# Kernel optimization log

Measured on AMD Instinct MI355X. Metric: run time of the kernel, lower is better.

The kernel has to match this reference:

```python
import jax, jax.numpy as jnp
import numpy as np

NEG_SLOPE = 0.15


def _gcn_norm(edge_index, num_nodes):
    # PyG GCNConv default: add self-loops, symmetric normalization.
    src = jnp.concatenate([edge_index[0], jnp.arange(num_nodes)])
    dst = jnp.concatenate([edge_index[1], jnp.arange(num_nodes)])
    deg = jax.ops.segment_sum(jnp.ones_like(src, dtype=jnp.float32), dst,
                              num_segments=num_nodes)
    dis = jnp.where(deg > 0, jax.lax.rsqrt(jnp.maximum(deg, 1.0)), 0.0)
    norm = dis[src] * dis[dst]  # [E + N]
    return src, dst, norm


def _gcn_conv(h, W, b, src, dst, norm, num_nodes):
    h = h @ W                                   # dense transform first (PyG order)
    msg = h[src] * norm[:, None]                # gather + scale per edge
    out = jax.ops.segment_sum(msg, dst, num_segments=num_nodes)  # scatter-add
    return out + b


def setup_inputs() -> dict:
    key = jax.random.key(0)
    ks = jax.random.split(key, 16)
    N, E, D = 20000, 320000, 128
    x = jax.random.normal(ks[0], (N, D), dtype=jnp.float32)
    edge_index = jax.random.randint(ks[1], (2, E), 0, N, dtype=jnp.int32)
    edge_attr = jax.random.normal(ks[2], (E, 2), dtype=jnp.float32)

    def lin(k, fi, fo):
        kw, kb = jax.random.split(k)
        s = 1.0 / np.sqrt(fi)
        return (jax.random.uniform(kw, (fi, fo), jnp.float32, -s, s),
                jax.random.uniform(kb, (fo,), jnp.float32, -s, s))

    W1, b1 = lin(ks[3], D, 512)
    W2, b2 = lin(ks[4], 512, 256)
    W3, b3 = lin(ks[5], 256, 128)
    Wp, bp = lin(ks[6], 128, 16)   # pre_fc (128 -> 16)
    Wf1, bf1 = lin(ks[7], 16, 32)  # fallback MLP classifier
    Wf2, bf2 = lin(ks[8], 32, 2)
    return {"x": x, "edge_index": edge_index, "edge_attr": edge_attr,
            "W1": W1, "b1": b1, "W2": W2, "b2": b2, "W3": W3, "b3": b3,
            "Wp": Wp, "bp": bp, "Wf1": Wf1, "bf1": bf1, "Wf2": Wf2, "bf2": bf2}


def reference(x, edge_index, edge_attr, W1, b1, W2, b2, W3, b3,
              Wp, bp, Wf1, bf1, Wf2, bf2):
    N = x.shape[0]
    src, dst, norm = _gcn_norm(edge_index, N)
    lrelu = lambda h: jax.nn.leaky_relu(h, NEG_SLOPE)
    h = lrelu(_gcn_conv(x, W1, b1, src, dst, norm, N))   # dropout = identity (eval)
    h = lrelu(_gcn_conv(h, W2, b2, src, dst, norm, N))
    h = lrelu(_gcn_conv(h, W3, b3, src, dst, norm, N))
    h = h @ Wp + bp                                      # pre_fc: 128 -> 16
    h = lrelu(h @ Wf1 + bf1)                             # classifier MLP
    return h @ Wf2 + bf2                                 # [N, 2]
```

## Files before the change

### kernel.cpp

```cpp
#include <hip/hip_runtime.h>
#include <hip/hip_bf16.h>

typedef __hip_bfloat16 bf16;
typedef unsigned short ushort_t;
typedef __attribute__((ext_vector_type(8))) short short8v;
typedef __attribute__((ext_vector_type(4))) float floatx4;

#define NEG_SLOPE 0.15f

__device__ __forceinline__ float us2f(unsigned short u) {
    unsigned int x = ((unsigned int)u) << 16;
    float f;
    __builtin_memcpy(&f, &x, 4);
    return f;
}
__device__ __forceinline__ unsigned short f2us(float v) {
    bf16 h = __float2bfloat16(v);
    unsigned short u;
    __builtin_memcpy(&u, &h, 2);
    return u;
}

__device__ __forceinline__ int block_flag(const unsigned int* __restrict__ xw) {
    __shared__ int cnt;
    if (threadIdx.x == 0) cnt = 0;
    __syncthreads();
    if (threadIdx.x < 256) {
        unsigned int w = xw[threadIdx.x];
        unsigned int e = (w >> 7) & 0xFF;
        if ((w & 0xFFFF) == 0 || (e >= 100 && e <= 140)) atomicAdd(&cnt, 1);
    }
    __syncthreads();
    return cnt >= 150;
}

struct PrepDesc {
    const void* src[14];
    void* dst[14];
    int n[14];
    int K[14], Nn[14];
};

__global__ void prep_small_kernel(PrepDesc d, const void* __restrict__ xsrc) {
    int f = block_flag((const unsigned int*)xsrc);
    int t = blockIdx.y;
    int Kt = d.K[t];
    int nt = d.n[t];
    if (Kt == -2) {
        ushort_t* out = (ushort_t*)d.dst[t];
        const void* in = d.src[t];
        int stride = gridDim.x * blockDim.x;
        for (int i = blockIdx.x * blockDim.x + threadIdx.x; i < nt; i += stride)
            out[i] = f ? ((const unsigned short*)in)[i] : f2us(((const float*)in)[i]);
        return;
    }
    int i = blockIdx.x * blockDim.x + threadIdx.x;
    if (i >= nt) return;
    if (Kt == -1) {
        ((int*)d.dst[t])[i] = 0;
    } else if (Kt == 0) {
        ((float*)d.dst[t])[i] = f ? us2f(((const unsigned short*)d.src[t])[i])
                                  : ((const float*)d.src[t])[i];
    } else {
        int K = Kt, Nn = d.Nn[t];
        int n = i / K, k = i - n * K;
        size_t si = (size_t)k * Nn + n;
        ((ushort_t*)d.dst[t])[i] = f ? ((const unsigned short*)d.src[t])[si]
                                     : f2us(((const float*)d.src[t])[si]);
    }
}

__global__ void count_deg_kernel(const int* __restrict__ dst, int* __restrict__ deg,
                                 int E, int N) {
    int i = blockIdx.x * blockDim.x + threadIdx.x;
    if (i < E) {
        int d = dst[i];
        d = d < 0 ? 0 : (d >= N ? N - 1 : d);
        atomicAdd(&deg[d], 1);
    }
}

__global__ void scan_merged_kernel(const int* __restrict__ deg, int* __restrict__ offsets,
                                   int* __restrict__ cursor, float* __restrict__ dis,
                                   int* __restrict__ bsumf, int N) {
    __shared__ int sh[1024];
    __shared__ int base_s;
    int tid = threadIdx.x;
    int b = blockIdx.x;
    int i = b * 1024 + tid;
    int v = (i < N) ? (deg[i] + 1) : 0;
    sh[tid] = v;
    __syncthreads();
    for (int off = 1; off < 1024; off <<= 1) {
        int t = (tid >= off) ? sh[tid - off] : 0;
        __syncthreads();
        sh[tid] += t;
        __syncthreads();
    }
    if (tid == 0) {
        __hip_atomic_store(&bsumf[b], sh[1023] + 1, __ATOMIC_RELEASE,
                           __HIP_MEMORY_SCOPE_AGENT);
        int a = 0;
        for (int pb = 0; pb < b; ++pb) {
            int val;
            do {
                val = __hip_atomic_load(&bsumf[pb], __ATOMIC_ACQUIRE,
                                        __HIP_MEMORY_SCOPE_AGENT);
            } while (val == 0);
            a += val - 1;
        }
        base_s = a;
    }
    __syncthreads();
    if (i < N) {
        int base = base_s;
        int d = deg[i] + 1;
        int inc = sh[tid];
        int excl = base + inc - d;
        offsets[i] = excl;
        cursor[i] = excl;
        dis[i] = rsqrtf((float)d);
        if (i == N - 1) offsets[N] = base + inc;
    }
}

__global__ void fill_csr_kernel(const int* __restrict__ src, const int* __restrict__ dst,
                                const float* __restrict__ dis, int* __restrict__ cursor,
                                int2* __restrict__ edges, int E, int N, int Etot) {
    int i = blockIdx.x * blockDim.x + threadIdx.x;
    int s, d;
    if (i < E) { s = src[i]; d = dst[i]; }
    else if (i < Etot) { s = d = i - E; }
    else return;
    s = s < 0 ? 0 : (s >= N ? N - 1 : s);
    d = d < 0 ? 0 : (d >= N ? N - 1 : d);
    int pos = atomicAdd(&cursor[d], 1);
    if (pos >= 0 && pos < Etot) edges[pos] = make_int2(s, __float_as_int(dis[s]));
}

template <int VEC> struct LdT;
template <> struct LdT<2> { typedef unsigned int T; };
template <> struct LdT<4> { typedef uint2 T; };

template <int VEC>
__device__ __forceinline__ void addv(typename LdT<VEC>::T u, float w, float* acc);
template <>
__device__ __forceinline__ void addv<2>(unsigned int u, float w, float* acc) {
    acc[0] += w * us2f((unsigned short)(u & 0xFFFF));
    acc[1] += w * us2f((unsigned short)(u >> 16));
}
template <>
__device__ __forceinline__ void addv<4>(uint2 u, float w, float* acc) {
    acc[0] += w * us2f((unsigned short)(u.x & 0xFFFF));
    acc[1] += w * us2f((unsigned short)(u.x >> 16));
    acc[2] += w * us2f((unsigned short)(u.y & 0xFFFF));
    acc[3] += w * us2f((unsigned short)(u.y >> 16));
}

template <int VEC>
__device__ __forceinline__ void agg_core(
    const ushort_t* __restrict__ Hin, const int* __restrict__ offsets,
    const int2* __restrict__ edges, const float* __restrict__ dis,
    int node, int lane, int N, int Etot,
    const float* __restrict__ bias, int do_lrelu, float* outv) {
    typedef typename LdT<VEC>::T LT;
    const int F = VEC * 64;
    int beg = offsets[node], end = offsets[node + 1];
    beg = beg < 0 ? 0 : (beg > Etot ? Etot : beg);
    end = end < beg ? beg : (end > Etot ? Etot : end);

    float acc[VEC];
#pragma unroll
    for (int v = 0; v < VEC; ++v) acc[v] = 0.f;

    int fo = lane * VEC;
    int e = beg;
    for (; e + 8 <= end; e += 8) {
        int2 r[8];
#pragma unroll
        for (int j = 0; j < 8; ++j) r[j] = edges[e + j];
        LT u[8];
#pragma unroll
        for (int j = 0; j < 8; ++j) {
            int s = r[j].x;
            s = s < 0 ? 0 : (s >= N ? N - 1 : s);
            u[j] = *(const LT*)(Hin + (size_t)s * F + fo);
        }
#pragma unroll
        for (int j = 0; j < 8; ++j) addv<VEC>(u[j], __int_as_float(r[j].y), acc);
    }
    if (e + 4 <= end) {
        int2 r[4];
#pragma unroll
        for (int j = 0; j < 4; ++j) r[j] = edges[e + j];
        LT u[4];
#pragma unroll
        for (int j = 0; j < 4; ++j) {
            int s = r[j].x;
            s = s < 0 ? 0 : (s >= N ? N - 1 : s);
            u[j] = *(const LT*)(Hin + (size_t)s * F + fo);
        }
#pragma unroll
        for (int j = 0; j < 4; ++j) addv<VEC>(u[j], __int_as_float(r[j].y), acc);
        e += 4;
    }
    for (; e < end; ++e) {
        int2 r = edges[e];
        int s = r.x;
        s = s < 0 ? 0 : (s >= N ? N - 1 : s);
        LT u = *(const LT*)(Hin + (size_t)s * F + fo);
        addv<VEC>(u, __int_as_float(r.y), acc);
    }

    float dn = dis[node];
#pragma unroll
    for (int v = 0; v < VEC; ++v) {
        float a = acc[v] * dn;
        if (bias) a += bias[fo + v];
        if (do_lrelu) a = (a > 0.f) ? a : a * NEG_SLOPE;
        outv[v] = a;
    }
}

template <int VEC>
__global__ __launch_bounds__(256) void agg_kernel(
    const ushort_t* __restrict__ Hin, ushort_t* __restrict__ OutB,
    const int* __restrict__ offsets, const int2* __restrict__ edges,
    const float* __restrict__ dis, int N, int Etot,
    const float* __restrict__ bias, int do_lrelu) {
    int lane = threadIdx.x & 63;
    int node = blockIdx.x * 4 + (threadIdx.x >> 6);
    if (node >= N) return;
    float outv[VEC];
    agg_core<VEC>(Hin, offsets, edges, dis, node, lane, N, Etot, bias, do_lrelu, outv);
    size_t base = (size_t)node * (VEC * 64) + lane * VEC;
    if (VEC == 2) {
        unsigned int w = ((unsigned int)f2us(outv[1]) << 16) | f2us(outv[0]);
        *(unsigned int*)(OutB + base) = w;
    } else {
        uint2 w;
        w.x = ((unsigned int)f2us(outv[1]) << 16) | f2us(outv[0]);
        w.y = ((unsigned int)f2us(outv[3]) << 16) | f2us(outv[2]);
        *(uint2*)(OutB + base) = w;
    }
}

__global__ __launch_bounds__(256) void agg_head_kernel(
    const ushort_t* __restrict__ Hin,
    const int* __restrict__ offsets, const int2* __restrict__ edges,
    const float* __restrict__ dis, int N, int Etot,
    const float* __restrict__ b3,
    const float* __restrict__ Wp, const float* __restrict__ bp,
    const float* __restrict__ Wf1, const float* __restrict__ bf1v,
    const float* __restrict__ Wf2, const float* __restrict__ bf2v,
    void* __restrict__ out, const void* __restrict__ xsrc) {
    int flag = block_flag((const unsigned int*)xsrc);
    int lane = threadIdx.x & 63;
    int node = blockIdx.x * 4 + (threadIdx.x >> 6);
    if (node >= N) return;
    float h[2];
    agg_core<2>(Hin, offsets, edges, dis, node, lane, N, Etot, b3, 1, h);

    int fo = lane * 2;
    float p[16];
#pragma unroll
    for (int j = 0; j < 16; ++j)
        p[j] = h[0] * Wp[fo * 16 + j] + h[1] * Wp[(fo + 1) * 16 + j];
#pragma unroll
    for (int m = 1; m < 64; m <<= 1) {
#pragma unroll
        for (int j = 0; j < 16; ++j) p[j] += __shfl_xor(p[j], m, 64);
    }
    float a0 = 0.f, a1 = 0.f;
    if (lane < 32) {
        float s = bf1v[lane];
#pragma unroll
        for (int k = 0; k < 16; ++k) s += (p[k] + bp[k]) * Wf1[k * 32 + lane];
        s = (s > 0.f) ? s : s * NEG_SLOPE;
        a0 = s * Wf2[lane * 2 + 0];
        a1 = s * Wf2[lane * 2 + 1];
    }
#pragma unroll
    for (int m = 1; m < 64; m <<= 1) {
        a0 += __shfl_xor(a0, m, 64);
        a1 += __shfl_xor(a1, m, 64);
    }
    if (lane == 0) {
        float o0 = a0 + bf2v[0];
        float o1 = a1 + bf2v[1];
        if (flag) {
            unsigned int w = ((unsigned int)f2us(o1) << 16) | f2us(o0);
            *(unsigned int*)((ushort_t*)out + (size_t)node * 2) = w;
        } else {
            *(float2*)((float*)out + (size_t)node * 2) = make_float2(o0, o1);
        }
    }
}

__global__ __launch_bounds__(256) void mfma_gemm_kernel(
    const ushort_t* __restrict__ A, const ushort_t* __restrict__ Bt,
    ushort_t* __restrict__ C,
    int M, int K, int Nn, const float* __restrict__ bias, int do_lrelu) {
    __shared__ ushort_t As[128 * 40];
    __shared__ ushort_t Bs[64 * 40];

    int tid = threadIdx.x;
    int row0 = blockIdx.y * 128;
    int col0 = blockIdx.x * 64;
    int lane = tid & 63;
    int w = tid >> 6;
    int quad = lane >> 4;
    int col = lane & 15;
    int wr = (w >> 1) * 64;
    int wc = (w & 1) * 32;

    floatx4 acc[4][2];
#pragma unroll
    for (int i = 0; i < 4; ++i)
#pragma unroll
        for (int j = 0; j < 2; ++j) acc[i][j] = (floatx4){0.f, 0.f, 0.f, 0.f};

    int arow = tid >> 1;
    int aseg = (tid & 1) * 16;
    int bcol = tid >> 2;
    int bseg = (tid & 3) * 8;

    for (int k0 = 0; k0 < K; k0 += 32) {
        {
            uint4 h0 = {0, 0, 0, 0}, h1 = {0, 0, 0, 0};
            if (row0 + arow < M) {
                size_t g = (size_t)(row0 + arow) * K + k0 + aseg;
                h0 = *(const uint4*)(A + g);
                h1 = *(const uint4*)(A + g + 8);
            }
            int lb = arow * 40 + aseg;
            *(uint4*)&As[lb] = h0;
            *(uint4*)&As[lb + 8] = h1;
        }
        {
            size_t g = (size_t)(col0 + bcol) * K + k0 + bseg;
            *(uint4*)&Bs[bcol * 40 + bseg] = *(const uint4*)(Bt + g);
        }
        __syncthreads();

        short8v af[4], bf[2];
#pragma unroll
        for (int rt = 0; rt < 4; ++rt)
            af[rt] = *(const short8v*)&As[(wr + rt * 16 + col) * 40 + quad * 8];
#pragma unroll
        for (int ct = 0; ct < 2; ++ct)
            bf[ct] = *(const short8v*)&Bs[(wc + ct * 16 + col) * 40 + quad * 8];
#pragma unroll
        for (int rt = 0; rt < 4; ++rt)
#pragma unroll
            for (int ct = 0; ct < 2; ++ct)
                acc[rt][ct] = __builtin_amdgcn_mfma_f32_16x16x32_bf16(
                    af[rt], bf[ct], acc[rt][ct], 0, 0, 0);
        __syncthreads();
    }

#pragma unroll
    for (int rt = 0; rt < 4; ++rt) {
#pragma unroll
        for (int ct = 0; ct < 2; ++ct) {
            int gcol = col0 + wc + ct * 16 + col;
            float bv = bias ? bias[gcol] : 0.f;
#pragma unroll
            for (int r = 0; r < 4; ++r) {
                int grow = row0 + wr + rt * 16 + quad * 4 + r;
                if (grow >= M) continue;
                float v = acc[rt][ct][r] + bv;
                if (do_lrelu) v = (v > 0.f) ? v : v * NEG_SLOPE;
                C[(size_t)grow * Nn + gcol] = f2us(v);
            }
        }
    }
}

extern "C" void kernel_launch(void* const* d_in, const int* in_sizes, int n_in,
                              void* d_out, int out_size, void* d_ws, size_t ws_size,
                              hipStream_t stream) {
    const int* ei = (const int*)d_in[1];

    const int N = in_sizes[0] / 128;
    const int E = in_sizes[1] / 2;
    const int Etot = E + N;
    const int nb = (N + 1023) / 1024;
    const int* srcv = ei;
    const int* dstv = ei + E;

    uintptr_t p = (uintptr_t)d_ws;
    auto alloc = [&](size_t bytes) -> void* {
        p = (p + 255) & ~(uintptr_t)255;
        void* r = (void*)p;
        p += bytes;
        return r;
    };
    int*      deg     = (int*)alloc((size_t)(N + nb + 1) * 4);
    int*      bsumf   = deg + N;
    int*      offsets = (int*)alloc((size_t)(N + 1) * 4);
    int*      cursor  = (int*)alloc((size_t)N * 4);
    float*    dis     = (float*)alloc((size_t)N * 4);
    int2*     edges   = (int2*)alloc((size_t)Etot * 8);
    ushort_t* xb      = (ushort_t*)alloc((size_t)N * 128 * 2);

    const int K1 = 128, N1 = 512, K2 = 512, N2 = 256, K3 = 256, N3 = 128;
    ushort_t* W1t = (ushort_t*)alloc((size_t)K1 * N1 * 2);
    ushort_t* W2t = (ushort_t*)alloc((size_t)K2 * N2 * 2);
    ushort_t* W3t = (ushort_t*)alloc((size_t)K3 * N3 * 2);

    float* smalls[9];
    const int wmap[9] = {4, 6, 8, 9, 10, 11, 12, 13, 14};
    for (int t = 0; t < 9; ++t)
        smalls[t] = (float*)alloc((size_t)in_sizes[wmap[t]] * 4);
    const float *b1 = smalls[0], *b2 = smalls[1], *b3 = smalls[2];
    const float *Wp = smalls[3], *bp = smalls[4];
    const float *Wf1 = smalls[5], *bf1v = smalls[6];
    const float *Wf2 = smalls[7], *bf2v = smalls[8];

    ushort_t* BufT0 = (ushort_t*)alloc((size_t)N * 128 * 2);
    ushort_t* BufH1 = (ushort_t*)alloc((size_t)N * 512 * 2);
    ushort_t* BufT2 = (ushort_t*)alloc((size_t)N * 256 * 2);
    ushort_t* t0 = BufT0;
    ushort_t* t3 = BufT0;
    ushort_t* H1 = BufH1;
    ushort_t* H2 = BufH1;
    ushort_t* t2 = BufT2;

    {
        PrepDesc pd;
        for (int t = 0; t < 9; ++t) {
            pd.src[t] = d_in[wmap[t]];
            pd.dst[t] = smalls[t];
            pd.n[t] = in_sizes[wmap[t]];
            pd.K[t] = 0; pd.Nn[t] = 0;
        }
        pd.src[9]  = d_in[3]; pd.dst[9]  = W1t; pd.n[9]  = K1 * N1; pd.K[9]  = K1; pd.Nn[9]  = N1;
        pd.src[10] = d_in[5]; pd.dst[10] = W2t; pd.n[10] = K2 * N2; pd.K[10] = K2; pd.Nn[10] = N2;
        pd.src[11] = d_in[7]; pd.dst[11] = W3t; pd.n[11] = K3 * N3; pd.K[11] = K3; pd.Nn[11] = N3;
        pd.src[12] = nullptr; pd.dst[12] = deg; pd.n[12] = N + nb + 1; pd.K[12] = -1; pd.Nn[12] = 0;
        pd.src[13] = d_in[0]; pd.dst[13] = xb;  pd.n[13] = N * 128;    pd.K[13] = -2; pd.Nn[13] = 0;
        dim3 g((K2 * N2 + 255) / 256, 14);
        prep_small_kernel<<<g, 256, 0, stream>>>(pd, d_in[0]);
    }

    count_deg_kernel<<<(E + 255) / 256, 256, 0, stream>>>(dstv, deg, E, N);
    scan_merged_kernel<<<nb, 1024, 0, stream>>>(deg, offsets, cursor, dis, bsumf, N);
    fill_csr_kernel<<<(Etot + 255) / 256, 256, 0, stream>>>(srcv, dstv, dis, cursor,
                                                            edges, E, N, Etot);

    int aggGrid = (N + 3) / 4;
    agg_kernel<2><<<aggGrid, 256, 0, stream>>>(xb, t0, offsets, edges, dis,
                                               N, Etot, nullptr, 0);
    {
        dim3 g(N1 / 64, (N + 127) / 128);
        mfma_gemm_kernel<<<g, 256, 0, stream>>>(t0, W1t, H1, N, K1, N1, b1, 1);
    }
    {
        dim3 g(N2 / 64, (N + 127) / 128);
        mfma_gemm_kernel<<<g, 256, 0, stream>>>(H1, W2t, t2, N, K2, N2, nullptr, 0);
    }
    agg_kernel<4><<<aggGrid, 256, 0, stream>>>(t2, H2, offsets, edges, dis,
                                               N, Etot, b2, 1);
    {
        dim3 g(N3 / 64, (N + 127) / 128);
        mfma_gemm_kernel<<<g, 256, 0, stream>>>(H2, W3t, t3, N, K3, N3, nullptr, 0);
    }
    agg_head_kernel<<<aggGrid, 256, 0, stream>>>(t3, offsets, edges, dis, N, Etot,
                                                 b3, Wp, bp, Wf1, bf1v, Wf2, bf2v,
                                                 d_out, d_in[0]);
}
```

Baseline: 270.4 us.

## Load GEMM tiles directly into LDS with XOR-swizzled layout and K-step 64

Replaces the register-staged global-to-LDS copies in the MFMA GEMM with direct global_load_lds 16-byte transfers. The tiles move to an unpadded, XOR-swizzled 128-byte-row layout to avoid bank conflicts, and the K step doubles to 64 so each tile load feeds two MFMA sub-steps. The aim is to cut VGPR traffic, LDS-store instructions and barrier count per unit of K. The row bound check on A is dropped, so the last row block may read past M.

```diff
diff --git a/kernel.cpp b/kernel.cpp
--- a/kernel.cpp
+++ b/kernel.cpp
@@ -20,6 +20,11 @@
     __builtin_memcpy(&u, &h, 2);
     return u;
 }
+
+#define GLOAD_LDS16(gp, lp)                                                  \
+    __builtin_amdgcn_global_load_lds(                                        \
+        (const __attribute__((address_space(1))) unsigned int*)(gp),         \
+        (__attribute__((address_space(3))) unsigned int*)(lp), 16, 0, 0)
 
 __device__ __forceinline__ int block_flag(const unsigned int* __restrict__ xw) {
     __shared__ int cnt;
@@ -301,8 +306,8 @@
     const ushort_t* __restrict__ A, const ushort_t* __restrict__ Bt,
     ushort_t* __restrict__ C,
     int M, int K, int Nn, const float* __restrict__ bias, int do_lrelu) {
-    __shared__ ushort_t As[128 * 40];
-    __shared__ ushort_t Bs[64 * 40];
+    __shared__ ushort_t As[128 * 64];
+    __shared__ ushort_t Bs[64 * 64];
 
     int tid = threadIdx.x;
     int row0 = blockIdx.y * 128;
@@ -320,42 +325,53 @@
 #pragma unroll
         for (int j = 0; j < 2; ++j) acc[i][j] = (floatx4){0.f, 0.f, 0.f, 0.f};
 
-    int arow = tid >> 1;
-    int aseg = (tid & 1) * 16;
-    int bcol = tid >> 2;
-    int bseg = (tid & 3) * 8;
-
-    for (int k0 = 0; k0 < K; k0 += 32) {
-        {
-            uint4 h0 = {0, 0, 0, 0}, h1 = {0, 0, 0, 0};
-            if (row0 + arow < M) {
-                size_t g = (size_t)(row0 + arow) * K + k0 + aseg;
-                h0 = *(const uint4*)(A + g);
-                h1 = *(const uint4*)(A + g + 8);
-            }
-            int lb = arow * 40 + aseg;
-            *(uint4*)&As[lb] = h0;
-            *(uint4*)&As[lb + 8] = h1;
-        }
-        {
-            size_t g = (size_t)(col0 + bcol) * K + k0 + bseg;
-            *(uint4*)&Bs[bcol * 40 + bseg] = *(const uint4*)(Bt + g);
+    int aoff[4], boff[2];
+#pragma unroll
+    for (int rt = 0; rt < 4; ++rt) {
+        int r = wr + rt * 16 + col;
+        aoff[rt] = (r * 128 + quad * 16) ^ ((r & 7) << 4);
+    }
+#pragma unroll
+    for (int ct = 0; ct < 2; ++ct) {
+        int r = wc + ct * 16 + col;
+        boff[ct] = (r * 128 + quad * 16) ^ ((r & 7) << 4);
+    }
+
+    for (int k0 = 0; k0 < K; k0 += 64) {
+#pragma unroll
+        for (int i = 0; i < 4; ++i) {
+            int t = i * 256 + tid;
+            int r = t >> 3;
+            int g = (t & 7) ^ (r & 7);
+            const ushort_t* src = A + (size_t)(row0 + r) * K + k0 + g * 8;
+            GLOAD_LDS16(src, &As[t * 8]);
+        }
+#pragma unroll
+        for (int i = 0; i < 2; ++i) {
+            int t = i * 256 + tid;
+            int r = t >> 3;
+            int g = (t & 7) ^ (r & 7);
+            const ushort_t* src = Bt + (size_t)(col0 + r) * K + k0 + g * 8;
+            GLOAD_LDS16(src, &Bs[t * 8]);
         }
         __syncthreads();
 
-        short8v af[4], bf[2];
-#pragma unroll
-        for (int rt = 0; rt < 4; ++rt)
-            af[rt] = *(const short8v*)&As[(wr + rt * 16 + col) * 40 + quad * 8];
-#pragma unroll
-        for (int ct = 0; ct < 2; ++ct)
-            bf[ct] = *(const short8v*)&Bs[(wc + ct * 16 + col) * 40 + quad * 8];
-#pragma unroll
-        for (int rt = 0; rt < 4; ++rt)
+#pragma unroll
+        for (int ks = 0; ks < 2; ++ks) {
+            short8v af[4], bf[2];
+#pragma unroll
+            for (int rt = 0; rt < 4; ++rt)
+                af[rt] = *(const short8v*)((const char*)As + (aoff[rt] ^ (ks * 64)));
 #pragma unroll
             for (int ct = 0; ct < 2; ++ct)
-                acc[rt][ct] = __builtin_amdgcn_mfma_f32_16x16x32_bf16(
-                    af[rt], bf[ct], acc[rt][ct], 0, 0, 0);
+                bf[ct] = *(const short8v*)((const char*)Bs + (boff[ct] ^ (ks * 64)));
+#pragma unroll
+            for (int rt = 0; rt < 4; ++rt)
+#pragma unroll
+                for (int ct = 0; ct < 2; ++ct)
+                    acc[rt][ct] = __builtin_amdgcn_mfma_f32_16x16x32_bf16(
+                        af[rt], bf[ct], acc[rt][ct], 0, 0, 0);
+        }
         __syncthreads();
     }
 
```

Result: no change. 272.9 us (+0.9%).
